# Kernel optimization log

Measured on AMD Instinct MI355X. Metric: run time of the kernel, lower is better.

The kernel has to match this reference:

```python
import jax, jax.numpy as jnp
import numpy as np

STRIDE = 1
PADDING = 1

def setup_inputs() -> dict:
    key = jax.random.key(0)
    k1, k2, k3 = jax.random.split(key, 3)
    N, C_in, H, W = 32, 128, 56, 56
    C_out, K = 256, 3
    inputs = jax.random.normal(k1, (N, C_in, H, W), dtype=jnp.float32)
    # trunc_normal(std=0.1) approximated by clipped normal
    filters = jnp.clip(jax.random.normal(k2, (C_out, C_in, K, K), dtype=jnp.float32) * 0.1, -0.2, 0.2)
    bias = jnp.clip(jax.random.normal(k3, (C_out,), dtype=jnp.float32) * 0.1, -0.2, 0.2)
    return {"inputs": inputs, "filters": filters, "bias": bias}

def reference(inputs, filters, bias):
    # Equivalent of the quadruple-loop conv: standard cross-correlation,
    # NCHW input, OIHW filters, stride/padding from module config.
    out = jax.lax.conv_general_dilated(
        inputs, filters,
        window_strides=(STRIDE, STRIDE),
        padding=[(PADDING, PADDING), (PADDING, PADDING)],
        dimension_numbers=("NCHW", "OIHW", "NCHW"),
    )
    out = out + bias[None, :, None, None]
    return out
```

## Files before the change

### kernel.cpp

```cpp
#include <hip/hip_runtime.h>

#define CIN    128
#define HH     56
#define WW_    56
#define NBATCH 32
#define COUT   256
#define KTOT   1152
#define PLANE  3136
#define HP     58
#define BM     128
#define BN     128
#define BK     64

#define WB_OFF   0
#define XP_OFF   (1u << 20)

typedef __attribute__((ext_vector_type(8))) short bf16x8;
typedef __attribute__((ext_vector_type(4))) float f32x4;

__device__ __forceinline__ unsigned short f2bf(float f) {
    unsigned int u = __builtin_bit_cast(unsigned int, f);
    u += 0x7fffu + ((u >> 16) & 1u);
    return (unsigned short)(u >> 16);
}

__device__ __forceinline__ void gl_lds16(const void* g, void* l) {
    __builtin_amdgcn_global_load_lds(
        (const __attribute__((address_space(1))) void*)g,
        (__attribute__((address_space(3))) void*)l, 16, 0, 0);
}

__global__ void wprep(const float* __restrict__ w, unsigned short* __restrict__ wb) {
    const int o = blockIdx.x;
    const int t = threadIdx.x;
    const float* src = w + (size_t)o * KTOT;
    unsigned short* dst = wb + (size_t)o * KTOT;
    #pragma unroll
    for (int e = 0; e < 5; ++e) {
        const int idx = t + e * 256;
        if (idx < KTOT) {
            const int ci  = idx / 9;
            const int tap = idx - ci * 9;
            dst[tap * 128 + ci] = f2bf(src[idx]);
        }
    }
}

__global__ __launch_bounds__(256)
void xprep(const float* __restrict__ in, unsigned short* __restrict__ xp) {
    const int b  = blockIdx.x;
    const int n  = b / HP;
    const int ho = b - n * HP;
    const int t  = threadIdx.x;
    uint4* orow = (uint4*)(xp + (((size_t)n * HP + ho) * HP) * CIN);

    if (ho == 0 || ho == HP - 1) {
        #pragma unroll
        for (int e = 0; e < 4; ++e) {
            const int idx = t + e * 256;
            if (idx < 928) orow[idx] = (uint4){0u, 0u, 0u, 0u};
        }
        return;
    }

    __shared__ unsigned short L[CIN * 57];
    const int h  = ho - 1;
    const int w  = t & 63;
    const int cb = t >> 6;
    if (w < WW_) {
        const float* ib = in + ((size_t)n * CIN) * PLANE + (size_t)h * WW_ + w;
        #pragma unroll
        for (int e = 0; e < 32; ++e) {
            const int ci = cb * 32 + e;
            L[ci * 57 + w] = f2bf(ib[(size_t)ci * PLANE]);
        }
    }
    __syncthreads();

    #pragma unroll
    for (int e = 0; e < 4; ++e) {
        const int idx = t + e * 256;
        if (idx < 928) {
            const int wo = idx >> 4;
            const int ch = idx & 15;
            uint4 pk = {0u, 0u, 0u, 0u};
            if (wo >= 1 && wo <= WW_) {
                const int wi = wo - 1;
                unsigned v[8];
                #pragma unroll
                for (int i = 0; i < 8; ++i)
                    v[i] = L[(ch * 8 + i) * 57 + wi];
                pk.x = v[0] | (v[1] << 16);
                pk.y = v[2] | (v[3] << 16);
                pk.z = v[4] | (v[5] << 16);
                pk.w = v[6] | (v[7] << 16);
            }
            orow[idx] = pk;
        }
    }
}

__global__ __launch_bounds__(256, 2)
void conv_mfma(const unsigned short* __restrict__ wb,
               const unsigned short* __restrict__ xp,
               const float* __restrict__ bias,
               float* __restrict__ out)
{
    __shared__ __align__(16) unsigned short Asm_[BM * BK];
    __shared__ __align__(16) unsigned short Bsm_[BN * BK];

    const int t    = threadIdx.x;
    const int pix0 = blockIdx.x * BN;
    const int c0   = blockIdx.y * BM;

    const int slot = t & 7;
    const int r32  = t >> 3;
    const int swiz = (slot ^ (r32 & 7)) * 16;

    const char* aBase = (const char*)wb + (size_t)(c0 + r32) * (KTOT * 2) + swiz;
    const char* bBase[4];
    #pragma unroll
    for (int p = 0; p < 4; ++p) {
        const int pix = pix0 + r32 + p * 32;
        const int n   = pix / PLANE;
        const int rem = pix - n * PLANE;
        const int h   = rem / WW_;
        const int w   = rem - h * WW_;
        bBase[p] = (const char*)xp + ((size_t)(n * HP + h) * HP + w) * (CIN * 2) + swiz;
    }

    const int lane = t & 63;
    const int wave = t >> 6;
    const int wm   = (wave & 1) * 64;
    const int wn   = (wave >> 1) * 64;
    const int lr   = lane & 15;
    const int quad = lane >> 4;
    const int rmod = lr & 7;

    f32x4 acc[4][4];
    #pragma unroll
    for (int i = 0; i < 4; ++i)
        #pragma unroll
        for (int j = 0; j < 4; ++j)
            acc[i][j] = (f32x4){0.f, 0.f, 0.f, 0.f};

    char* const asmb = (char*)Asm_;
    char* const bsmb = (char*)Bsm_;

    for (int tap = 0; tap < 9; ++tap) {
        const int toff = ((tap / 3) * HP + (tap % 3)) * (CIN * 2);
        for (int ci0b = 0; ci0b < 256; ci0b += 128) {
            const int abyte = tap * 256 + ci0b;
            #pragma unroll
            for (int p = 0; p < 4; ++p)
                gl_lds16(aBase + (size_t)p * 32 * (KTOT * 2) + abyte, asmb + p * 4096 + t * 16);
            #pragma unroll
            for (int p = 0; p < 4; ++p)
                gl_lds16(bBase[p] + toff + ci0b, bsmb + p * 4096 + t * 16);
            __syncthreads();

            #pragma unroll
            for (int kk = 0; kk < 2; ++kk) {
                bf16x8 af[4], bfr[4];
                #pragma unroll
                for (int i = 0; i < 4; ++i) {
                    const int r = wm + i * 16 + lr;
                    const int phys = ((kk * 4 + quad) ^ rmod) * 16;
                    af[i] = *(const bf16x8*)(asmb + r * 128 + phys);
                }
                #pragma unroll
                for (int j = 0; j < 4; ++j) {
                    const int r = wn + j * 16 + lr;
                    const int phys = ((kk * 4 + quad) ^ rmod) * 16;
                    bfr[j] = *(const bf16x8*)(bsmb + r * 128 + phys);
                }
                #pragma unroll
                for (int i = 0; i < 4; ++i)
                    #pragma unroll
                    for (int j = 0; j < 4; ++j)
                        acc[i][j] = __builtin_amdgcn_mfma_f32_16x16x32_bf16(af[i], bfr[j], acc[i][j], 0, 0, 0);
            }
            __syncthreads();
        }
    }

    #pragma unroll
    for (int j = 0; j < 4; ++j) {
        const int pg    = pix0 + wn + j * 16 + lr;
        const int ni    = pg / PLANE;
        const int inner = pg - ni * PLANE;
        float* op = out + (size_t)ni * (COUT * PLANE) + inner;
        #pragma unroll
        for (int i = 0; i < 4; ++i) {
            const int crow = c0 + wm + i * 16 + quad * 4;
            #pragma unroll
            for (int r = 0; r < 4; ++r)
                op[(size_t)(crow + r) * PLANE] = acc[i][j][r] + bias[crow + r];
        }
    }
}

extern "C" void kernel_launch(void* const* d_in, const int* in_sizes, int n_in,
                              void* d_out, int out_size, void* d_ws, size_t ws_size,
                              hipStream_t stream) {
    const float* in   = (const float*)d_in[0];
    const float* wt   = (const float*)d_in[1];
    const float* bias = (const float*)d_in[2];
    float* out        = (float*)d_out;

    unsigned short* wb = (unsigned short*)((char*)d_ws + WB_OFF);
    unsigned short* xp = (unsigned short*)((char*)d_ws + XP_OFF);

    wprep<<<COUT, 256, 0, stream>>>(wt, wb);
    xprep<<<NBATCH * HP, 256, 0, stream>>>(in, xp);

    dim3 grid((NBATCH * PLANE) / BN, COUT / BM);
    conv_mfma<<<grid, 256, 0, stream>>>(wb, xp, bias, out);
}
```

Before: 207.4 us.

## Triple-buffer conv GEMM with 256x128 tiles, 512 threads and async prefetch

The conv kernel now computes all 256 output channels per block with 8 waves, so each input tile loaded into LDS is used by every channel and is not fetched twice. It uses a three-stage LDS ring of global_load_lds copies issued two K-tiles ahead, with explicit vmcnt waits, barriers and setprio around the MFMA bursts to overlap loads with compute. The weight-prep kernel is also vectorised through shared memory. LDS grows to 144KB per block, which limits occupancy, and the hand-counted waitcnt logic is fragile.

```diff
diff --git a/kernel.cpp b/kernel.cpp
--- a/kernel.cpp
+++ b/kernel.cpp
@@ -8,12 +8,17 @@
 #define KTOT   1152
 #define PLANE  3136
 #define HP     58
-#define BM     128
+#define BM     256
 #define BN     128
-#define BK     64
+#define NTILE  18
 
 #define WB_OFF   0
 #define XP_OFF   (1u << 20)
+
+#define ABUF_BYTES 32768
+#define BBUF_BYTES 16384
+#define BUF_STRIDE (ABUF_BYTES + BBUF_BYTES)
+#define LDS_BYTES  (3 * BUF_STRIDE)
 
 typedef __attribute__((ext_vector_type(8))) short bf16x8;
 typedef __attribute__((ext_vector_type(4))) float f32x4;
@@ -30,20 +35,29 @@
         (__attribute__((address_space(3))) void*)l, 16, 0, 0);
 }
 
-__global__ void wprep(const float* __restrict__ w, unsigned short* __restrict__ wb) {
+__global__ __launch_bounds__(256)
+void wprep(const float* __restrict__ w, unsigned short* __restrict__ wb) {
+    __shared__ __align__(16) unsigned short L[KTOT];
     const int o = blockIdx.x;
     const int t = threadIdx.x;
-    const float* src = w + (size_t)o * KTOT;
-    unsigned short* dst = wb + (size_t)o * KTOT;
-    #pragma unroll
-    for (int e = 0; e < 5; ++e) {
-        const int idx = t + e * 256;
-        if (idx < KTOT) {
-            const int ci  = idx / 9;
-            const int tap = idx - ci * 9;
-            dst[tap * 128 + ci] = f2bf(src[idx]);
-        }
-    }
+    const float4* src = (const float4*)(w + (size_t)o * KTOT);
+    #pragma unroll
+    for (int e = 0; e < 2; ++e) {
+        const int q = t + e * 256;
+        if (q < 288) {
+            const float4 v = src[q];
+            #pragma unroll
+            for (int u = 0; u < 4; ++u) {
+                const int idx = q * 4 + u;
+                const int ci  = idx / 9;
+                const int tap = idx - ci * 9;
+                L[tap * 128 + ci] = f2bf(((const float*)&v)[u]);
+            }
+        }
+    }
+    __syncthreads();
+    if (t < 144)
+        ((uint4*)(wb + (size_t)o * KTOT))[t] = ((const uint4*)L)[t];
 }
 
 __global__ __launch_bounds__(256)
@@ -100,39 +114,37 @@
     }
 }
 
-__global__ __launch_bounds__(256, 2)
+__global__ __launch_bounds__(512, 2)
 void conv_mfma(const unsigned short* __restrict__ wb,
                const unsigned short* __restrict__ xp,
                const float* __restrict__ bias,
                float* __restrict__ out)
 {
-    __shared__ __align__(16) unsigned short Asm_[BM * BK];
-    __shared__ __align__(16) unsigned short Bsm_[BN * BK];
+    extern __shared__ __align__(16) char lds[];
 
     const int t    = threadIdx.x;
     const int pix0 = blockIdx.x * BN;
-    const int c0   = blockIdx.y * BM;
 
     const int slot = t & 7;
-    const int r32  = t >> 3;
-    const int swiz = (slot ^ (r32 & 7)) * 16;
-
-    const char* aBase = (const char*)wb + (size_t)(c0 + r32) * (KTOT * 2) + swiz;
-    const char* bBase[4];
-    #pragma unroll
-    for (int p = 0; p < 4; ++p) {
-        const int pix = pix0 + r32 + p * 32;
+    const int r    = t >> 3;
+    const int swz  = (slot ^ (r & 7)) * 16;
+
+    const char* aBase = (const char*)wb + (size_t)r * (KTOT * 2) + swz;
+    const char* bBase[2];
+    #pragma unroll
+    for (int p = 0; p < 2; ++p) {
+        const int pix = pix0 + r + p * 64;
         const int n   = pix / PLANE;
         const int rem = pix - n * PLANE;
         const int h   = rem / WW_;
         const int w   = rem - h * WW_;
-        bBase[p] = (const char*)xp + ((size_t)(n * HP + h) * HP + w) * (CIN * 2) + swiz;
+        bBase[p] = (const char*)xp + ((size_t)(n * HP + h) * HP + w) * (CIN * 2) + swz;
     }
 
     const int lane = t & 63;
     const int wave = t >> 6;
-    const int wm   = (wave & 1) * 64;
-    const int wn   = (wave >> 1) * 64;
+    const int wm   = (wave >> 1) * 64;
+    const int wn   = (wave & 1) * 64;
     const int lr   = lane & 15;
     const int quad = lane >> 4;
     const int rmod = lr & 7;
@@ -144,44 +156,79 @@
         for (int j = 0; j < 4; ++j)
             acc[i][j] = (f32x4){0.f, 0.f, 0.f, 0.f};
 
-    char* const asmb = (char*)Asm_;
-    char* const bsmb = (char*)Bsm_;
-
-    for (int tap = 0; tap < 9; ++tap) {
-        const int toff = ((tap / 3) * HP + (tap % 3)) * (CIN * 2);
-        for (int ci0b = 0; ci0b < 256; ci0b += 128) {
-            const int abyte = tap * 256 + ci0b;
-            #pragma unroll
-            for (int p = 0; p < 4; ++p)
-                gl_lds16(aBase + (size_t)p * 32 * (KTOT * 2) + abyte, asmb + p * 4096 + t * 16);
-            #pragma unroll
-            for (int p = 0; p < 4; ++p)
-                gl_lds16(bBase[p] + toff + ci0b, bsmb + p * 4096 + t * 16);
-            __syncthreads();
-
-            #pragma unroll
-            for (int kk = 0; kk < 2; ++kk) {
-                bf16x8 af[4], bfr[4];
-                #pragma unroll
-                for (int i = 0; i < 4; ++i) {
-                    const int r = wm + i * 16 + lr;
-                    const int phys = ((kk * 4 + quad) ^ rmod) * 16;
-                    af[i] = *(const bf16x8*)(asmb + r * 128 + phys);
-                }
-                #pragma unroll
-                for (int j = 0; j < 4; ++j) {
-                    const int r = wn + j * 16 + lr;
-                    const int phys = ((kk * 4 + quad) ^ rmod) * 16;
-                    bfr[j] = *(const bf16x8*)(bsmb + r * 128 + phys);
-                }
-                #pragma unroll
-                for (int i = 0; i < 4; ++i)
-                    #pragma unroll
-                    for (int j = 0; j < 4; ++j)
-                        acc[i][j] = __builtin_amdgcn_mfma_f32_16x16x32_bf16(af[i], bfr[j], acc[i][j], 0, 0, 0);
-            }
-            __syncthreads();
-        }
+    auto stage = [&](int kt, int part) {
+        char* ab = lds + (kt % 3) * BUF_STRIDE;
+        char* bb = ab + ABUF_BYTES;
+        const int tap   = kt >> 1;
+        const int ci0b  = (kt & 1) << 7;
+        const int abyte = tap * 256 + ci0b;
+        const int toff  = ((tap / 3) * HP + (tap % 3)) * (CIN * 2) + ci0b;
+        if (part == 0) {
+            gl_lds16(aBase + (size_t)0 * 64 * (KTOT * 2) + abyte, ab + 0 * 8192 + t * 16);
+            gl_lds16(aBase + (size_t)1 * 64 * (KTOT * 2) + abyte, ab + 1 * 8192 + t * 16);
+            gl_lds16(bBase[0] + toff,                             bb + 0 * 8192 + t * 16);
+        } else {
+            gl_lds16(aBase + (size_t)2 * 64 * (KTOT * 2) + abyte, ab + 2 * 8192 + t * 16);
+            gl_lds16(aBase + (size_t)3 * 64 * (KTOT * 2) + abyte, ab + 3 * 8192 + t * 16);
+            gl_lds16(bBase[1] + toff,                             bb + 1 * 8192 + t * 16);
+        }
+    };
+
+    stage(0, 0); stage(0, 1);
+    stage(1, 0); stage(1, 1);
+    asm volatile("s_waitcnt vmcnt(6)" ::: "memory");
+    __builtin_amdgcn_s_barrier();
+
+    for (int kt = 0; kt < NTILE; ++kt) {
+        const char* ab = lds + (kt % 3) * BUF_STRIDE;
+        const char* bb = ab + ABUF_BYTES;
+        bf16x8 af[4], bfr[4];
+
+        {
+            const int phys = (quad ^ rmod) * 16;
+            #pragma unroll
+            for (int i = 0; i < 4; ++i)
+                af[i] = *(const bf16x8*)(ab + (wm + i * 16 + lr) * 128 + phys);
+            #pragma unroll
+            for (int j = 0; j < 4; ++j)
+                bfr[j] = *(const bf16x8*)(bb + (wn + j * 16 + lr) * 128 + phys);
+        }
+        if (kt + 2 < NTILE) stage(kt + 2, 0);
+        __builtin_amdgcn_s_barrier();
+        asm volatile("s_waitcnt lgkmcnt(0)" ::: "memory");
+        __builtin_amdgcn_sched_barrier(0);
+        __builtin_amdgcn_s_setprio(1);
+        #pragma unroll
+        for (int i = 0; i < 4; ++i)
+            #pragma unroll
+            for (int j = 0; j < 4; ++j)
+                acc[i][j] = __builtin_amdgcn_mfma_f32_16x16x32_bf16(af[i], bfr[j], acc[i][j], 0, 0, 0);
+        __builtin_amdgcn_s_setprio(0);
+        __builtin_amdgcn_s_barrier();
+
+        {
+            const int phys = ((4 + quad) ^ rmod) * 16;
+            #pragma unroll
+            for (int i = 0; i < 4; ++i)
+                af[i] = *(const bf16x8*)(ab + (wm + i * 16 + lr) * 128 + phys);
+            #pragma unroll
+            for (int j = 0; j < 4; ++j)
+                bfr[j] = *(const bf16x8*)(bb + (wn + j * 16 + lr) * 128 + phys);
+        }
+        if (kt + 2 < NTILE) stage(kt + 2, 1);
+        __builtin_amdgcn_s_barrier();
+        asm volatile("s_waitcnt lgkmcnt(0)" ::: "memory");
+        __builtin_amdgcn_sched_barrier(0);
+        __builtin_amdgcn_s_setprio(1);
+        #pragma unroll
+        for (int i = 0; i < 4; ++i)
+            #pragma unroll
+            for (int j = 0; j < 4; ++j)
+                acc[i][j] = __builtin_amdgcn_mfma_f32_16x16x32_bf16(af[i], bfr[j], acc[i][j], 0, 0, 0);
+        __builtin_amdgcn_s_setprio(0);
+        if (kt + 2 < NTILE)      asm volatile("s_waitcnt vmcnt(6)" ::: "memory");
+        else if (kt + 1 < NTILE) asm volatile("s_waitcnt vmcnt(0)" ::: "memory");
+        __builtin_amdgcn_s_barrier();
     }
 
     #pragma unroll
@@ -192,10 +239,10 @@
         float* op = out + (size_t)ni * (COUT * PLANE) + inner;
         #pragma unroll
         for (int i = 0; i < 4; ++i) {
-            const int crow = c0 + wm + i * 16 + quad * 4;
-            #pragma unroll
-            for (int r = 0; r < 4; ++r)
-                op[(size_t)(crow + r) * PLANE] = acc[i][j][r] + bias[crow + r];
+            const int crow = wm + i * 16 + quad * 4;
+            #pragma unroll
+            for (int rr = 0; rr < 4; ++rr)
+                op[(size_t)(crow + rr) * PLANE] = acc[i][j][rr] + bias[crow + rr];
         }
     }
 }
@@ -208,12 +255,14 @@
     const float* bias = (const float*)d_in[2];
     float* out        = (float*)d_out;
 
-    unsigned short* wb = (unsigned short*)((char*)d_ws + WB_OFF);
-    unsigned short* xp = (unsigned short*)((char*)d_ws + XP_OFF);
-
-    wprep<<<COUT, 256, 0, stream>>>(wt, wb);
-    xprep<<<NBATCH * HP, 256, 0, stream>>>(in, xp);
-
-    dim3 grid((NBATCH * PLANE) / BN, COUT / BM);
-    conv_mfma<<<grid, 256, 0, stream>>>(wb, xp, bias, out);
-}
+    unsigned short* wbuf = (unsigned short*)((char*)d_ws + WB_OFF);
+    unsigned short* xpb  = (unsigned short*)((char*)d_ws + XP_OFF);
+
+    (void)hipFuncSetAttribute((const void*)conv_mfma,
+                              hipFuncAttributeMaxDynamicSharedMemorySize, LDS_BYTES);
+
+    wprep<<<COUT, 256, 0, stream>>>(wt, wbuf);
+    xprep<<<NBATCH * HP, 256, 0, stream>>>(in, xpb);
+
+    conv_mfma<<<dim3((NBATCH * PLANE) / BN), 512, LDS_BYTES, stream>>>(wbuf, xpb, bias, out);
+}
```

After: 220.2 us. 6.2% more time.

## Software-pipeline conv GEMM with 4-slot LDS ring and register double-buffering

Applied to the files above, without the earlier changes.

Restructures the MFMA conv main loop into 36 K-steps of 32 channels each. A 4-slot dynamic-LDS ring is prefetched three steps ahead with global_load_lds, and LDS-to-register fragments are double-buffered. Fine-grained vmcnt waits replace the two full __syncthreads per iteration, and s_setprio raises priority around the MFMA bursts. It also flattens the grid with an XCD-aware block remap pairing the two output-channel tiles, and vectorises the weight-prep kernel through LDS. The 64KB of LDS per block may lower occupancy, and the hand-written waitcnt logic risks correctness.

```diff
diff --git a/kernel.cpp b/kernel.cpp
--- a/kernel.cpp
+++ b/kernel.cpp
@@ -10,10 +10,13 @@
 #define HP     58
 #define BM     128
 #define BN     128
-#define BK     64
+#define NSTEP  36
 
 #define WB_OFF   0
 #define XP_OFF   (1u << 20)
+
+#define SLOT_BYTES 16384
+#define LDS_BYTES  (4 * SLOT_BYTES)
 
 typedef __attribute__((ext_vector_type(8))) short bf16x8;
 typedef __attribute__((ext_vector_type(4))) float f32x4;
@@ -30,20 +33,29 @@
         (__attribute__((address_space(3))) void*)l, 16, 0, 0);
 }
 
-__global__ void wprep(const float* __restrict__ w, unsigned short* __restrict__ wb) {
+__global__ __launch_bounds__(256)
+void wprep(const float* __restrict__ w, unsigned short* __restrict__ wb) {
+    __shared__ __align__(16) unsigned short L[KTOT];
     const int o = blockIdx.x;
     const int t = threadIdx.x;
-    const float* src = w + (size_t)o * KTOT;
-    unsigned short* dst = wb + (size_t)o * KTOT;
-    #pragma unroll
-    for (int e = 0; e < 5; ++e) {
-        const int idx = t + e * 256;
-        if (idx < KTOT) {
-            const int ci  = idx / 9;
-            const int tap = idx - ci * 9;
-            dst[tap * 128 + ci] = f2bf(src[idx]);
-        }
-    }
+    const float4* src = (const float4*)(w + (size_t)o * KTOT);
+    #pragma unroll
+    for (int e = 0; e < 2; ++e) {
+        const int q = t + e * 256;
+        if (q < 288) {
+            const float4 v = src[q];
+            #pragma unroll
+            for (int u = 0; u < 4; ++u) {
+                const int idx = q * 4 + u;
+                const int ci  = idx / 9;
+                const int tap = idx - ci * 9;
+                L[tap * 128 + ci] = f2bf(((const float*)&v)[u]);
+            }
+        }
+    }
+    __syncthreads();
+    if (t < 144)
+        ((uint4*)(wb + (size_t)o * KTOT))[t] = ((const uint4*)L)[t];
 }
 
 __global__ __launch_bounds__(256)
@@ -106,28 +118,46 @@
                const float* __restrict__ bias,
                float* __restrict__ out)
 {
-    __shared__ __align__(16) unsigned short Asm_[BM * BK];
-    __shared__ __align__(16) unsigned short Bsm_[BN * BK];
-
-    const int t    = threadIdx.x;
-    const int pix0 = blockIdx.x * BN;
-    const int c0   = blockIdx.y * BM;
-
-    const int slot = t & 7;
-    const int r32  = t >> 3;
-    const int swiz = (slot ^ (r32 & 7)) * 16;
-
-    const char* aBase = (const char*)wb + (size_t)(c0 + r32) * (KTOT * 2) + swiz;
-    const char* bBase[4];
-    #pragma unroll
-    for (int p = 0; p < 4; ++p) {
-        const int pix = pix0 + r32 + p * 32;
+    extern __shared__ __align__(16) char lds[];
+
+    const int t = threadIdx.x;
+
+    const int bid0 = blockIdx.x;
+    const int bid  = (bid0 & 7) * ((NBATCH * PLANE / BN * 2) >> 3) + (bid0 >> 3);
+    const int c0   = (bid & 1) * BM;
+    const int pix0 = (bid >> 1) * BN;
+
+    const char* aSrc[2]; const char* bSrc[2];
+    int aDst[2], bDst[2];
+    #pragma unroll
+    for (int e = 0; e < 2; ++e) {
+        const int idx  = t + e * 256;
+        const int line = idx >> 3;
+        const int us   = (idx & 7) ^ (line & 7);
+        const int row  = 2 * line + (us >> 2);
+        const int koff = (us & 3) * 16;
+        aSrc[e] = (const char*)wb + (size_t)(c0 + row) * (KTOT * 2) + koff;
+        const int pix = pix0 + row;
         const int n   = pix / PLANE;
         const int rem = pix - n * PLANE;
         const int h   = rem / WW_;
         const int w   = rem - h * WW_;
-        bBase[p] = (const char*)xp + ((size_t)(n * HP + h) * HP + w) * (CIN * 2) + swiz;
-    }
+        bSrc[e] = (const char*)xp + ((size_t)(n * HP + h) * HP + w) * (CIN * 2) + koff;
+        aDst[e] = idx * 16;
+        bDst[e] = 8192 + idx * 16;
+    }
+
+    auto stage = [&](int hi) {
+        char* slot = lds + (hi & 3) * SLOT_BYTES;
+        const int tap  = hi >> 2;
+        const int q    = hi & 3;
+        const int aoff = tap * 256 + q * 64;
+        const int boff = ((tap / 3) * HP + (tap % 3)) * (CIN * 2) + q * 64;
+        gl_lds16(aSrc[0] + aoff, slot + aDst[0]);
+        gl_lds16(aSrc[1] + aoff, slot + aDst[1]);
+        gl_lds16(bSrc[0] + boff, slot + bDst[0]);
+        gl_lds16(bSrc[1] + boff, slot + bDst[1]);
+    };
 
     const int lane = t & 63;
     const int wave = t >> 6;
@@ -135,7 +165,22 @@
     const int wn   = (wave >> 1) * 64;
     const int lr   = lane & 15;
     const int quad = lane >> 4;
-    const int rmod = lr & 7;
+    int offA[4], offB[4];
+    #pragma unroll
+    for (int i = 0; i < 4; ++i) {
+        const int ra = wm + i * 16 + lr;
+        offA[i] = (ra >> 1) * 128 + ((((ra & 1) * 4 + quad) ^ ((ra >> 1) & 7)) * 16);
+        const int rb = wn + i * 16 + lr;
+        offB[i] = 8192 + (rb >> 1) * 128 + ((((rb & 1) * 4 + quad) ^ ((rb >> 1) & 7)) * 16);
+    }
+
+    auto ldreg = [&](int hi, bf16x8 (&fr)[8]) {
+        const char* slot = lds + (hi & 3) * SLOT_BYTES;
+        #pragma unroll
+        for (int i = 0; i < 4; ++i) fr[i]     = *(const bf16x8*)(slot + offA[i]);
+        #pragma unroll
+        for (int i = 0; i < 4; ++i) fr[4 + i] = *(const bf16x8*)(slot + offB[i]);
+    };
 
     f32x4 acc[4][4];
     #pragma unroll
@@ -144,45 +189,46 @@
         for (int j = 0; j < 4; ++j)
             acc[i][j] = (f32x4){0.f, 0.f, 0.f, 0.f};
 
-    char* const asmb = (char*)Asm_;
-    char* const bsmb = (char*)Bsm_;
-
-    for (int tap = 0; tap < 9; ++tap) {
-        const int toff = ((tap / 3) * HP + (tap % 3)) * (CIN * 2);
-        for (int ci0b = 0; ci0b < 256; ci0b += 128) {
-            const int abyte = tap * 256 + ci0b;
+    auto domfma = [&](bf16x8 (&fr)[8]) {
+        __builtin_amdgcn_s_setprio(1);
+        #pragma unroll
+        for (int i = 0; i < 4; ++i)
             #pragma unroll
-            for (int p = 0; p < 4; ++p)
-                gl_lds16(aBase + (size_t)p * 32 * (KTOT * 2) + abyte, asmb + p * 4096 + t * 16);
-            #pragma unroll
-            for (int p = 0; p < 4; ++p)
-                gl_lds16(bBase[p] + toff + ci0b, bsmb + p * 4096 + t * 16);
-            __syncthreads();
-
-            #pragma unroll
-            for (int kk = 0; kk < 2; ++kk) {
-                bf16x8 af[4], bfr[4];
-                #pragma unroll
-                for (int i = 0; i < 4; ++i) {
-                    const int r = wm + i * 16 + lr;
-                    const int phys = ((kk * 4 + quad) ^ rmod) * 16;
-                    af[i] = *(const bf16x8*)(asmb + r * 128 + phys);
-                }
-                #pragma unroll
-                for (int j = 0; j < 4; ++j) {
-                    const int r = wn + j * 16 + lr;
-                    const int phys = ((kk * 4 + quad) ^ rmod) * 16;
-                    bfr[j] = *(const bf16x8*)(bsmb + r * 128 + phys);
-                }
-                #pragma unroll
-                for (int i = 0; i < 4; ++i)
-                    #pragma unroll
-                    for (int j = 0; j < 4; ++j)
-                        acc[i][j] = __builtin_amdgcn_mfma_f32_16x16x32_bf16(af[i], bfr[j], acc[i][j], 0, 0, 0);
-            }
-            __syncthreads();
-        }
-    }
+            for (int j = 0; j < 4; ++j)
+                acc[i][j] = __builtin_amdgcn_mfma_f32_16x16x32_bf16(fr[i], fr[4 + j], acc[i][j], 0, 0, 0);
+        __builtin_amdgcn_s_setprio(0);
+    };
+
+    auto step = [&](int hi, bf16x8 (&cur)[8], bf16x8 (&nxt)[8]) {
+        asm volatile("s_waitcnt vmcnt(4)" ::: "memory");
+        __builtin_amdgcn_s_barrier();
+        asm volatile("s_waitcnt lgkmcnt(0)" ::: "memory");
+        __builtin_amdgcn_sched_barrier(0);
+        ldreg(hi + 1, nxt);
+        if (hi + 3 < NSTEP) stage(hi + 3);
+        domfma(cur);
+    };
+
+    stage(0); stage(1); stage(2);
+    asm volatile("s_waitcnt vmcnt(8)" ::: "memory");
+    __builtin_amdgcn_s_barrier();
+
+    bf16x8 fA[8], fB[8];
+    ldreg(0, fA);
+
+    for (int h2 = 0; h2 < NSTEP - 2; h2 += 2) {
+        step(h2,     fA, fB);
+        step(h2 + 1, fB, fA);
+    }
+    asm volatile("s_waitcnt vmcnt(0)" ::: "memory");
+    __builtin_amdgcn_s_barrier();
+    asm volatile("s_waitcnt lgkmcnt(0)" ::: "memory");
+    __builtin_amdgcn_sched_barrier(0);
+    ldreg(35, fB);
+    domfma(fA);
+    asm volatile("s_waitcnt lgkmcnt(0)" ::: "memory");
+    __builtin_amdgcn_sched_barrier(0);
+    domfma(fB);
 
     #pragma unroll
     for (int j = 0; j < 4; ++j) {
@@ -208,12 +254,14 @@
     const float* bias = (const float*)d_in[2];
     float* out        = (float*)d_out;
 
-    unsigned short* wb = (unsigned short*)((char*)d_ws + WB_OFF);
-    unsigned short* xp = (unsigned short*)((char*)d_ws + XP_OFF);
-
-    wprep<<<COUT, 256, 0, stream>>>(wt, wb);
-    xprep<<<NBATCH * HP, 256, 0, stream>>>(in, xp);
-
-    dim3 grid((NBATCH * PLANE) / BN, COUT / BM);
-    conv_mfma<<<grid, 256, 0, stream>>>(wb, xp, bias, out);
-}
+    unsigned short* wbuf = (unsigned short*)((char*)d_ws + WB_OFF);
+    unsigned short* xpb  = (unsigned short*)((char*)d_ws + XP_OFF);
+
+    (void)hipFuncSetAttribute((const void*)conv_mfma,
+                              hipFuncAttributeMaxDynamicSharedMemorySize, LDS_BYTES);
+
+    wprep<<<COUT, 256, 0, stream>>>(wt, wbuf);
+    xprep<<<NBATCH * HP, 256, 0, stream>>>(in, xpb);
+
+    conv_mfma<<<dim3((NBATCH * PLANE / BN) * 2), 256, LDS_BYTES, stream>>>(wbuf, xpb, bias, out);
+}
```

Measured after the change: 212.7 us. 2.5% more time.
